# Kernel tuning notes

Measured on AMD Instinct MI355X. Metric: run time of the kernel, lower is better.

Reference implementation:

```python
import jax, jax.numpy as jnp
import numpy as np

B, T, D, F, E, TOPK = 4, 2048, 1024, 2752, 8, 2


def setup_inputs() -> dict:
    key = jax.random.key(0)
    k1, k2, k3, k4 = jax.random.split(key, 4)
    x = jax.random.normal(k1, (B, T, D), dtype=jnp.float32)
    # Expert params, torch Linear(bias=False) stored as [in, out] for x @ W
    W13 = jax.random.normal(k2, (E, D, 2 * F), dtype=jnp.float32) * 0.02  # gate+up packed
    W2 = jax.random.normal(k3, (E, F, D), dtype=jnp.float32) * 0.02       # down proj
    Wr = jax.random.normal(k4, (D, E), dtype=jnp.float32) * 0.02          # router
    return {"x": x, "W13": W13, "W2": W2, "Wr": Wr}


def reference(x, W13, W2, Wr):
    b, t, d = x.shape
    xf = x.reshape(-1, d)                       # [N, D]
    n = xf.shape[0]
    logits = xf @ Wr                            # [N, E]
    probs = jax.nn.softmax(logits, axis=-1)
    top_probs, top_idx = jax.lax.top_k(probs, TOPK)  # [N, K]
    top_probs = top_probs / top_probs.sum(axis=-1, keepdims=True)
    # combine weights: cw[n, e] = sum_k top_probs[n, k] * (top_idx[n, k] == e)
    cw = jnp.zeros((n, E), dtype=xf.dtype).at[jnp.arange(n)[:, None], top_idx].add(top_probs)
    out = jnp.zeros_like(xf)
    for e in range(E):  # small fixed expert loop; tokens with cw==0 contribute nothing
        x13 = xf @ W13[e]                       # [N, 2F]
        x1, x3 = jnp.split(x13, 2, axis=-1)
        h = jax.nn.silu(x1) * x3                # SwiGLU
        out = out + cw[:, e:e + 1] * (h @ W2[e])
    return out.reshape(b, t, d)
```

## Files before the change

kernel.cpp:

```cpp
#include <hip/hip_runtime.h>
#include <stdint.h>

#define NTOK 8192
#define DDIM 1024
#define FDIM 2752
#define NEXP 8
#define DF2  5504
#define NSLOT 16384

typedef __attribute__((ext_vector_type(8))) short bf16x8;
typedef __attribute__((ext_vector_type(4))) float f32x4;
typedef __attribute__((ext_vector_type(4))) unsigned short u16x4;
typedef __attribute__((ext_vector_type(8))) unsigned short u16x8;

constexpr size_t XB_OFF   = 0;
constexpr size_t XB_SZ    = (size_t)NTOK * DDIM * 2;
constexpr size_t W13T_OFF = XB_OFF + XB_SZ;
constexpr size_t W13T_SZ  = (size_t)NEXP * DF2 * DDIM * 2;
constexpr size_t W2T_OFF  = W13T_OFF + W13T_SZ;
constexpr size_t W2T_SZ   = (size_t)NEXP * DDIM * FDIM * 2;
constexpr size_t H_OFF    = W2T_OFF + W2T_SZ;
constexpr size_t H_SZ     = (size_t)NSLOT * FDIM * 2;
constexpr size_t ST_OFF   = H_OFF + H_SZ;
constexpr size_t SW_OFF   = ST_OFF + (size_t)NSLOT * 4;
constexpr size_t TTI_OFF  = SW_OFF + (size_t)NSLOT * 4;
constexpr size_t TTW_OFF  = TTI_OFF + (size_t)NTOK * 8;
constexpr size_t META_OFF = TTW_OFF + (size_t)NTOK * 8;

__device__ __forceinline__ unsigned short f2bf(float f) {
  unsigned u = __float_as_uint(f);
  u += 0x7FFFu + ((u >> 16) & 1u);
  return (unsigned short)(u >> 16);
}

__device__ __forceinline__ void gl_lds16(const void* g, void* l) {
  __builtin_amdgcn_global_load_lds(
      (const __attribute__((address_space(1))) unsigned int*)g,
      (__attribute__((address_space(3))) unsigned int*)l, 16, 0, 0);
}

__global__ void cvt_x_k(const float* __restrict__ x, unsigned short* __restrict__ xb) {
  int i = blockIdx.x * 256 + threadIdx.x;
  float4 v = ((const float4*)x)[i];
  u16x4 o;
  o[0] = f2bf(v.x); o[1] = f2bf(v.y); o[2] = f2bf(v.z); o[3] = f2bf(v.w);
  ((u16x4*)xb)[i] = o;
}

__global__ void tcvt_k(const float* __restrict__ src, unsigned short* __restrict__ dst,
                       int R, int C) {
  __shared__ unsigned short tile[64][65];
  long base = (long)blockIdx.z * R * C;
  src += base; dst += base;
  int r0 = blockIdx.y * 64, c0 = blockIdx.x * 64;
  int t = threadIdx.x;
  int rr = t >> 4, cc = (t & 15) * 4;
  for (int i = 0; i < 4; ++i) {
    float4 v = *(const float4*)&src[(long)(r0 + rr + i * 16) * C + c0 + cc];
    tile[rr + i * 16][cc + 0] = f2bf(v.x);
    tile[rr + i * 16][cc + 1] = f2bf(v.y);
    tile[rr + i * 16][cc + 2] = f2bf(v.z);
    tile[rr + i * 16][cc + 3] = f2bf(v.w);
  }
  __syncthreads();
  int dr = t >> 2, sg = (t & 3) * 16;
  u16x8 o0, o1;
  for (int i = 0; i < 8; ++i) { o0[i] = tile[sg + i][dr]; o1[i] = tile[sg + 8 + i][dr]; }
  unsigned short* dp = &dst[(long)(c0 + dr) * R + r0 + sg];
  *(u16x8*)dp = o0;
  *(u16x8*)(dp + 8) = o1;
}

__global__ void router_k(const float* __restrict__ x, const float* __restrict__ Wr,
                         int* __restrict__ meta, int2* __restrict__ tt_i,
                         float2* __restrict__ tt_w) {
  int lane = threadIdx.x & 63;
  int tok = blockIdx.x * 4 + (threadIdx.x >> 6);
  float acc[8];
#pragma unroll
  for (int e = 0; e < 8; ++e) acc[e] = 0.f;
  const float4* xr = (const float4*)(x + (long)tok * DDIM);
#pragma unroll
  for (int it = 0; it < 4; ++it) {
    float4 v = xr[it * 64 + lane];
    int d = (it * 64 + lane) * 4;
    float xv[4] = {v.x, v.y, v.z, v.w};
#pragma unroll
    for (int j = 0; j < 4; ++j) {
      const float4* wr = (const float4*)(Wr + (long)(d + j) * NEXP);
      float4 wa = wr[0], wb = wr[1];
      acc[0] += xv[j] * wa.x; acc[1] += xv[j] * wa.y;
      acc[2] += xv[j] * wa.z; acc[3] += xv[j] * wa.w;
      acc[4] += xv[j] * wb.x; acc[5] += xv[j] * wb.y;
      acc[6] += xv[j] * wb.z; acc[7] += xv[j] * wb.w;
    }
  }
#pragma unroll
  for (int e = 0; e < 8; ++e)
    for (int off = 32; off; off >>= 1) acc[e] += __shfl_xor(acc[e], off, 64);
  if (lane == 0) {
    float m = acc[0];
    for (int e = 1; e < 8; ++e) m = fmaxf(m, acc[e]);
    float p[8];
    for (int e = 0; e < 8; ++e) p[e] = __expf(acc[e] - m);
    int e0 = 0;
    for (int e = 1; e < 8; ++e) if (p[e] > p[e0]) e0 = e;
    int e1 = -1;
    for (int e = 0; e < 8; ++e) { if (e == e0) continue; if (e1 < 0 || p[e] > p[e1]) e1 = e; }
    float s = p[e0] + p[e1];
    atomicAdd(&meta[e0], 1);
    atomicAdd(&meta[e1], 1);
    tt_i[tok] = make_int2(e0, e1);
    tt_w[tok] = make_float2(p[e0] / s, p[e1] / s);
  }
}

__global__ void offsets_k(int* meta) {
  int run = 0;
  for (int e = 0; e < NEXP; ++e) { meta[16 + e] = run; run += meta[e]; }
}

__global__ void scatter_k(const int2* __restrict__ tt_i, const float2* __restrict__ tt_w,
                          int* __restrict__ meta, int* __restrict__ slot_tok,
                          float* __restrict__ slot_w) {
  int n = blockIdx.x * 256 + threadIdx.x;
  int2 ei = tt_i[n];
  float2 wv = tt_w[n];
  int p0 = atomicAdd(&meta[8 + ei.x], 1);
  int s0 = meta[16 + ei.x] + p0;
  slot_tok[s0] = n; slot_w[s0] = wv.x;
  int p1 = atomicAdd(&meta[8 + ei.y], 1);
  int s1 = meta[16 + ei.y] + p1;
  slot_tok[s1] = n; slot_w[s1] = wv.y;
}

__global__ __launch_bounds__(256) void gemm1_k(
    const unsigned short* __restrict__ xb, const unsigned short* __restrict__ w13t,
    const int* __restrict__ meta, const int* __restrict__ slot_tok,
    unsigned short* __restrict__ h) {
  int e = blockIdx.z;
  int n_e = meta[e];
  int m0 = blockIdx.y * 128;
  if (m0 >= n_e) return;
  int base = meta[16 + e];
  int c0 = blockIdx.x * 64;
  const unsigned short* wB = w13t + (long)e * DF2 * DDIM;

  __shared__ unsigned short Al[128 * 32];
  __shared__ unsigned short B1l[64 * 32];
  __shared__ unsigned short B2l[64 * 32];

  int t = threadIdx.x;
  int lane = t & 63, w = t >> 6;
  int wm = w & 1, wn = w >> 1;
  int ar0 = t >> 2, ac = (t & 3) * 8;

  int tokA0 = slot_tok[base + min(m0 + ar0, n_e - 1)];
  int tokA1 = slot_tok[base + min(m0 + 64 + ar0, n_e - 1)];
  const unsigned short* gA0 = xb + (long)tokA0 * DDIM + ac;
  const unsigned short* gA1 = xb + (long)tokA1 * DDIM + ac;
  const unsigned short* gB1 = wB + (long)(c0 + ar0) * DDIM + ac;
  const unsigned short* gB2 = gB1 + (long)FDIM * DDIM;

  unsigned short* lA0 = &Al[t * 8];
  unsigned short* lA1 = &Al[(t + 256) * 8];
  unsigned short* lB1 = &B1l[t * 8];
  unsigned short* lB2 = &B2l[t * 8];

  f32x4 accg[4][2], accu[4][2];
#pragma unroll
  for (int mi = 0; mi < 4; ++mi)
#pragma unroll
    for (int ni = 0; ni < 2; ++ni) {
      accg[mi][ni] = (f32x4){0.f, 0.f, 0.f, 0.f};
      accu[mi][ni] = (f32x4){0.f, 0.f, 0.f, 0.f};
    }

  for (int k0 = 0; k0 < DDIM; k0 += 32) {
    gl_lds16(gA0 + k0, lA0);
    gl_lds16(gA1 + k0, lA1);
    gl_lds16(gB1 + k0, lB1);
    gl_lds16(gB2 + k0, lB2);
    __syncthreads();
    int q8 = (lane >> 4) * 8;
    bf16x8 a[4], b1[2], b2[2];
#pragma unroll
    for (int mi = 0; mi < 4; ++mi)
      a[mi] = *(const bf16x8*)&Al[(wm * 64 + mi * 16 + (lane & 15)) * 32 + q8];
#pragma unroll
    for (int ni = 0; ni < 2; ++ni) {
      b1[ni] = *(const bf16x8*)&B1l[(wn * 32 + ni * 16 + (lane & 15)) * 32 + q8];
      b2[ni] = *(const bf16x8*)&B2l[(wn * 32 + ni * 16 + (lane & 15)) * 32 + q8];
    }
#pragma unroll
    for (int mi = 0; mi < 4; ++mi)
#pragma unroll
      for (int ni = 0; ni < 2; ++ni) {
        accg[mi][ni] = __builtin_amdgcn_mfma_f32_16x16x32_bf16(a[mi], b1[ni], accg[mi][ni], 0, 0, 0);
        accu[mi][ni] = __builtin_amdgcn_mfma_f32_16x16x32_bf16(a[mi], b2[ni], accu[mi][ni], 0, 0, 0);
      }
    __syncthreads();
  }
  int quad = lane >> 4;
  int col0 = c0 + wn * 32 + (lane & 15);
#pragma unroll
  for (int mi = 0; mi < 4; ++mi)
#pragma unroll
    for (int r = 0; r < 4; ++r) {
      int m = m0 + wm * 64 + mi * 16 + quad * 4 + r;
      if (m < n_e) {
        unsigned short* hp = &h[(long)(base + m) * FDIM + col0];
#pragma unroll
        for (int ni = 0; ni < 2; ++ni) {
          float g = accg[mi][ni][r], u = accu[mi][ni][r];
          float hv = (g / (1.f + __expf(-g))) * u;
          hp[ni * 16] = f2bf(hv);
        }
      }
    }
}

__global__ __launch_bounds__(256) void gemm2_k(
    const unsigned short* __restrict__ h, const unsigned short* __restrict__ w2t,
    const int* __restrict__ meta, const int* __restrict__ slot_tok,
    const float* __restrict__ slot_w, float* __restrict__ out) {
  int e = blockIdx.z;
  int n_e = meta[e];
  int m0 = blockIdx.y * 128;
  if (m0 >= n_e) return;
  int base = meta[16 + e];
  int n0 = blockIdx.x * 128;
  const unsigned short* wB = w2t + (long)e * DDIM * FDIM;

  __shared__ unsigned short Al[128 * 32];
  __shared__ unsigned short Bl[128 * 32];

  int t = threadIdx.x;
  int lane = t & 63, w = t >> 6;
  int wm = w & 1, wn = w >> 1;
  int ar0 = t >> 2, ac = (t & 3) * 8;

  int rA0 = base + min(m0 + ar0, n_e - 1);
  int rA1 = base + min(m0 + 64 + ar0, n_e - 1);
  const unsigned short* gA0 = h + (long)rA0 * FDIM + ac;
  const unsigned short* gA1 = h + (long)rA1 * FDIM + ac;
  const unsigned short* gB0 = wB + (long)(n0 + ar0) * FDIM + ac;
  const unsigned short* gB1 = gB0 + (long)64 * FDIM;

  unsigned short* lA0 = &Al[t * 8];
  unsigned short* lA1 = &Al[(t + 256) * 8];
  unsigned short* lB0 = &Bl[t * 8];
  unsigned short* lB1 = &Bl[(t + 256) * 8];

  f32x4 acc[4][4];
#pragma unroll
  for (int mi = 0; mi < 4; ++mi)
#pragma unroll
    for (int ni = 0; ni < 4; ++ni) acc[mi][ni] = (f32x4){0.f, 0.f, 0.f, 0.f};

  for (int k0 = 0; k0 < FDIM; k0 += 32) {
    gl_lds16(gA0 + k0, lA0);
    gl_lds16(gA1 + k0, lA1);
    gl_lds16(gB0 + k0, lB0);
    gl_lds16(gB1 + k0, lB1);
    __syncthreads();
    int q8 = (lane >> 4) * 8;
    bf16x8 a[4], b[4];
#pragma unroll
    for (int mi = 0; mi < 4; ++mi)
      a[mi] = *(const bf16x8*)&Al[(wm * 64 + mi * 16 + (lane & 15)) * 32 + q8];
#pragma unroll
    for (int ni = 0; ni < 4; ++ni)
      b[ni] = *(const bf16x8*)&Bl[(wn * 64 + ni * 16 + (lane & 15)) * 32 + q8];
#pragma unroll
    for (int mi = 0; mi < 4; ++mi)
#pragma unroll
      for (int ni = 0; ni < 4; ++ni)
        acc[mi][ni] = __builtin_amdgcn_mfma_f32_16x16x32_bf16(a[mi], b[ni], acc[mi][ni], 0, 0, 0);
    __syncthreads();
  }
  int quad = lane >> 4;
#pragma unroll
  for (int mi = 0; mi < 4; ++mi)
#pragma unroll
    for (int r = 0; r < 4; ++r) {
      int m = m0 + wm * 64 + mi * 16 + quad * 4 + r;
      if (m < n_e) {
        int tok = slot_tok[base + m];
        float wgt = slot_w[base + m];
        float* op = out + (long)tok * DDIM + n0 + wn * 64 + (lane & 15);
#pragma unroll
        for (int ni = 0; ni < 4; ++ni) atomicAdd(op + ni * 16, wgt * acc[mi][ni][r]);
      }
    }
}

extern "C" void kernel_launch(void* const* d_in, const int* in_sizes, int n_in,
                              void* d_out, int out_size, void* d_ws, size_t ws_size,
                              hipStream_t stream) {
  const float* x   = (const float*)d_in[0];
  const float* W13 = (const float*)d_in[1];
  const float* W2  = (const float*)d_in[2];
  const float* Wr  = (const float*)d_in[3];
  float* out = (float*)d_out;
  char* ws = (char*)d_ws;

  unsigned short* xb   = (unsigned short*)(ws + XB_OFF);
  unsigned short* w13t = (unsigned short*)(ws + W13T_OFF);
  unsigned short* w2t  = (unsigned short*)(ws + W2T_OFF);
  unsigned short* hbuf = (unsigned short*)(ws + H_OFF);
  int*    slot_tok = (int*)(ws + ST_OFF);
  float*  slot_w   = (float*)(ws + SW_OFF);
  int2*   tt_i     = (int2*)(ws + TTI_OFF);
  float2* tt_w     = (float2*)(ws + TTW_OFF);
  int*    meta     = (int*)(ws + META_OFF);

  hipMemsetAsync(d_out, 0, (size_t)NTOK * DDIM * sizeof(float), stream);
  hipMemsetAsync(meta, 0, 128, stream);

  cvt_x_k<<<NTOK * DDIM / 4 / 256, 256, 0, stream>>>(x, xb);
  tcvt_k<<<dim3(DF2 / 64, DDIM / 64, NEXP), 256, 0, stream>>>(W13, w13t, DDIM, DF2);
  tcvt_k<<<dim3(DDIM / 64, FDIM / 64, NEXP), 256, 0, stream>>>(W2, w2t, FDIM, DDIM);
  router_k<<<NTOK / 4, 256, 0, stream>>>(x, Wr, meta, tt_i, tt_w);
  offsets_k<<<1, 1, 0, stream>>>(meta);
  scatter_k<<<NTOK / 256, 256, 0, stream>>>(tt_i, tt_w, meta, slot_tok, slot_w);
  gemm1_k<<<dim3(FDIM / 64, NTOK / 128, NEXP), 256, 0, stream>>>(xb, w13t, meta, slot_tok, hbuf);
  gemm2_k<<<dim3(DDIM / 128, NTOK / 128, NEXP), 256, 0, stream>>>(hbuf, w2t, meta, slot_tok, slot_w, out);
}
```

Baseline: 1.108 ms.

## Replace atomic scatter-add with per-slot output buffer and combine kernel; reorder GEMM grids

gemm2 now writes unweighted per-slot results into a dense fp32 buffer, aliased onto the no-longer-needed W13 transpose region, instead of doing weighted float atomicAdds into the output. A new combine kernel gathers each token's two slot rows and applies the router weights, which also removes the output memset. Both GEMM grids swap their x and y roles so that blocks sharing a weight column tile are launched next to each other, aiming for better L2 reuse of weights. The cost is an extra 64MB write and read through the intermediate buffer plus one more kernel launch.

```diff
diff --git a/kernel.cpp b/kernel.cpp
--- a/kernel.cpp
+++ b/kernel.cpp
@@ -22,8 +22,8 @@
 constexpr size_t H_OFF    = W2T_OFF + W2T_SZ;
 constexpr size_t H_SZ     = (size_t)NSLOT * FDIM * 2;
 constexpr size_t ST_OFF   = H_OFF + H_SZ;
-constexpr size_t SW_OFF   = ST_OFF + (size_t)NSLOT * 4;
-constexpr size_t TTI_OFF  = SW_OFF + (size_t)NSLOT * 4;
+constexpr size_t TS_OFF   = ST_OFF + (size_t)NSLOT * 4;
+constexpr size_t TTI_OFF  = TS_OFF + (size_t)NSLOT * 4;
 constexpr size_t TTW_OFF  = TTI_OFF + (size_t)NTOK * 8;
 constexpr size_t META_OFF = TTW_OFF + (size_t)NTOK * 8;
 
@@ -122,16 +122,15 @@
 
 __global__ void scatter_k(const int2* __restrict__ tt_i, const float2* __restrict__ tt_w,
                           int* __restrict__ meta, int* __restrict__ slot_tok,
-                          float* __restrict__ slot_w) {
+                          int* __restrict__ tok_slot) {
   int n = blockIdx.x * 256 + threadIdx.x;
   int2 ei = tt_i[n];
-  float2 wv = tt_w[n];
   int p0 = atomicAdd(&meta[8 + ei.x], 1);
   int s0 = meta[16 + ei.x] + p0;
-  slot_tok[s0] = n; slot_w[s0] = wv.x;
+  slot_tok[s0] = n; tok_slot[2 * n] = s0;
   int p1 = atomicAdd(&meta[8 + ei.y], 1);
   int s1 = meta[16 + ei.y] + p1;
-  slot_tok[s1] = n; slot_w[s1] = wv.y;
+  slot_tok[s1] = n; tok_slot[2 * n + 1] = s1;
 }
 
 __global__ __launch_bounds__(256) void gemm1_k(
@@ -140,10 +139,10 @@
     unsigned short* __restrict__ h) {
   int e = blockIdx.z;
   int n_e = meta[e];
-  int m0 = blockIdx.y * 128;
+  int m0 = blockIdx.x * 128;
   if (m0 >= n_e) return;
   int base = meta[16 + e];
-  int c0 = blockIdx.x * 64;
+  int c0 = blockIdx.y * 64;
   const unsigned short* wB = w13t + (long)e * DF2 * DDIM;
 
   __shared__ unsigned short Al[128 * 32];
@@ -222,14 +221,13 @@
 
 __global__ __launch_bounds__(256) void gemm2_k(
     const unsigned short* __restrict__ h, const unsigned short* __restrict__ w2t,
-    const int* __restrict__ meta, const int* __restrict__ slot_tok,
-    const float* __restrict__ slot_w, float* __restrict__ out) {
+    const int* __restrict__ meta, float* __restrict__ y) {
   int e = blockIdx.z;
   int n_e = meta[e];
-  int m0 = blockIdx.y * 128;
+  int m0 = blockIdx.x * 128;
   if (m0 >= n_e) return;
   int base = meta[16 + e];
-  int n0 = blockIdx.x * 128;
+  int n0 = blockIdx.y * 128;
   const unsigned short* wB = w2t + (long)e * DDIM * FDIM;
 
   __shared__ unsigned short Al[128 * 32];
@@ -286,13 +284,27 @@
     for (int r = 0; r < 4; ++r) {
       int m = m0 + wm * 64 + mi * 16 + quad * 4 + r;
       if (m < n_e) {
-        int tok = slot_tok[base + m];
-        float wgt = slot_w[base + m];
-        float* op = out + (long)tok * DDIM + n0 + wn * 64 + (lane & 15);
-#pragma unroll
-        for (int ni = 0; ni < 4; ++ni) atomicAdd(op + ni * 16, wgt * acc[mi][ni][r]);
+        float* yp = y + (long)(base + m) * DDIM + n0 + wn * 64 + (lane & 15);
+#pragma unroll
+        for (int ni = 0; ni < 4; ++ni) yp[ni * 16] = acc[mi][ni][r];
       }
     }
+}
+
+__global__ void combine_k(const float* __restrict__ y, const int* __restrict__ tok_slot,
+                          const float2* __restrict__ tt_w, float* __restrict__ out) {
+  int i = blockIdx.x * 256 + threadIdx.x;
+  int tok = i >> 8, c = i & 255;
+  int s0 = tok_slot[2 * tok], s1 = tok_slot[2 * tok + 1];
+  float2 wv = tt_w[tok];
+  float4 a = ((const float4*)(y + (long)s0 * DDIM))[c];
+  float4 b = ((const float4*)(y + (long)s1 * DDIM))[c];
+  float4 o;
+  o.x = wv.x * a.x + wv.y * b.x;
+  o.y = wv.x * a.y + wv.y * b.y;
+  o.z = wv.x * a.z + wv.y * b.z;
+  o.w = wv.x * a.w + wv.y * b.w;
+  ((float4*)(out + (long)tok * DDIM))[c] = o;
 }
 
 extern "C" void kernel_launch(void* const* d_in, const int* in_sizes, int n_in,
@@ -309,13 +321,13 @@
   unsigned short* w13t = (unsigned short*)(ws + W13T_OFF);
   unsigned short* w2t  = (unsigned short*)(ws + W2T_OFF);
   unsigned short* hbuf = (unsigned short*)(ws + H_OFF);
+  float*  ybuf     = (float*)(ws + W13T_OFF);
   int*    slot_tok = (int*)(ws + ST_OFF);
-  float*  slot_w   = (float*)(ws + SW_OFF);
+  int*    tok_slot = (int*)(ws + TS_OFF);
   int2*   tt_i     = (int2*)(ws + TTI_OFF);
   float2* tt_w     = (float2*)(ws + TTW_OFF);
   int*    meta     = (int*)(ws + META_OFF);
 
-  hipMemsetAsync(d_out, 0, (size_t)NTOK * DDIM * sizeof(float), stream);
   hipMemsetAsync(meta, 0, 128, stream);
 
   cvt_x_k<<<NTOK * DDIM / 4 / 256, 256, 0, stream>>>(x, xb);
@@ -323,7 +335,8 @@
   tcvt_k<<<dim3(DDIM / 64, FDIM / 64, NEXP), 256, 0, stream>>>(W2, w2t, FDIM, DDIM);
   router_k<<<NTOK / 4, 256, 0, stream>>>(x, Wr, meta, tt_i, tt_w);
   offsets_k<<<1, 1, 0, stream>>>(meta);
-  scatter_k<<<NTOK / 256, 256, 0, stream>>>(tt_i, tt_w, meta, slot_tok, slot_w);
-  gemm1_k<<<dim3(FDIM / 64, NTOK / 128, NEXP), 256, 0, stream>>>(xb, w13t, meta, slot_tok, hbuf);
-  gemm2_k<<<dim3(DDIM / 128, NTOK / 128, NEXP), 256, 0, stream>>>(hbuf, w2t, meta, slot_tok, slot_w, out);
-}
+  scatter_k<<<NTOK / 256, 256, 0, stream>>>(tt_i, tt_w, meta, slot_tok, tok_slot);
+  gemm1_k<<<dim3(64, FDIM / 64, NEXP), 256, 0, stream>>>(xb, w13t, meta, slot_tok, hbuf);
+  gemm2_k<<<dim3(64, DDIM / 128, NEXP), 256, 0, stream>>>(hbuf, w2t, meta, ybuf);
+  combine_k<<<NTOK * DDIM / 4 / 256, 256, 0, stream>>>(ybuf, tok_slot, tt_w, out);
+}
```

Result: slower. 1.380 ms (+24.6%).
